# Kernel optimization log

Hardware: AMD Instinct MI355X
Metric: run time of the kernel (lower is better)

The kernel has to match this reference:

```python
import jax, jax.numpy as jnp
import numpy as np

D_MODEL = 1024
NUM_HEADS = 16
HEAD_DIM = D_MODEL // NUM_HEADS
FFN_HIDDEN = 4096
EPS = 1e-5


def setup_inputs() -> dict:
    key = jax.random.key(0)
    ks = jax.random.split(key, 7)
    s = 0.02
    return {
        "x": jax.random.normal(ks[0], (2, 2048, D_MODEL), dtype=jnp.float32),
        "W_qkv": jax.random.normal(ks[1], (D_MODEL, 3 * D_MODEL), dtype=jnp.float32) * s,
        "b_qkv": jnp.zeros((3 * D_MODEL,), dtype=jnp.float32),
        "W_o": jax.random.normal(ks[2], (D_MODEL, D_MODEL), dtype=jnp.float32) * s,
        "b_o": jnp.zeros((D_MODEL,), dtype=jnp.float32),
        "gamma1": jnp.ones((D_MODEL,), dtype=jnp.float32),
        "beta1": jnp.zeros((D_MODEL,), dtype=jnp.float32),
        "W1": jax.random.normal(ks[3], (D_MODEL, FFN_HIDDEN), dtype=jnp.float32) * s,
        "b1": jnp.zeros((FFN_HIDDEN,), dtype=jnp.float32),
        "W2": jax.random.normal(ks[4], (FFN_HIDDEN, D_MODEL), dtype=jnp.float32) * s,
        "b2": jnp.zeros((D_MODEL,), dtype=jnp.float32),
        "gamma2": jnp.ones((D_MODEL,), dtype=jnp.float32),
        "beta2": jnp.zeros((D_MODEL,), dtype=jnp.float32),
    }


def _layernorm(x, gamma, beta):
    mean = jnp.mean(x, axis=-1, keepdims=True)
    var = jnp.mean((x - mean) ** 2, axis=-1, keepdims=True)
    return gamma * (x - mean) / jnp.sqrt(var + EPS) + beta


def reference(x, W_qkv, b_qkv, W_o, b_o, gamma1, beta1, W1, b1, W2, b2, gamma2, beta2):
    B, S, D = x.shape
    # ---- multi-head attention ----
    qkv = x @ W_qkv + b_qkv                       # [B,S,3D]
    qkv = qkv.reshape(B, S, NUM_HEADS, 3 * HEAD_DIM).transpose(0, 2, 1, 3)  # [B,H,S,3hd]
    q, k, v = jnp.split(qkv, 3, axis=-1)          # each [B,H,S,hd]
    scores = jnp.einsum("bhqd,bhkd->bhqk", q, k) / np.sqrt(HEAD_DIM)
    attn = jax.nn.softmax(scores, axis=-1)
    vals = jnp.einsum("bhqk,bhkd->bhqd", attn, v)
    vals = vals.transpose(0, 2, 1, 3).reshape(B, S, D)
    attn_out = vals @ W_o + b_o
    # dropout disabled (eval mode)
    h = _layernorm(attn_out + x, gamma1, beta1)
    # ---- position-wise FFN (dropout before relu per source, disabled) ----
    ffn = jax.nn.relu(h @ W1 + b1) @ W2 + b2
    return _layernorm(ffn + h, gamma2, beta2)
```

## Files before the change

kernel.cpp:

```cpp
#include <hip/hip_runtime.h>
#include <stdint.h>

typedef float v4f __attribute__((ext_vector_type(4)));
typedef __bf16 v8bf __attribute__((ext_vector_type(8)));
typedef __bf16 v4bf __attribute__((ext_vector_type(4)));
typedef unsigned short v8us __attribute__((ext_vector_type(8)));
typedef unsigned short v4us __attribute__((ext_vector_type(4)));

__device__ __forceinline__ float b2f(unsigned short u) {
    union { float f; uint32_t i; } x; x.i = ((uint32_t)u) << 16; return x.f;
}
__device__ __forceinline__ unsigned short f2b(float f) {
    union { float f; uint32_t u; } x; x.f = f;
    uint32_t r = x.u + 0x7fffu + ((x.u >> 16) & 1u);
    return (unsigned short)(r >> 16);
}

__device__ __forceinline__ void gload16(const unsigned short* g, unsigned short* l) {
    __builtin_amdgcn_global_load_lds(
        (const __attribute__((address_space(1))) void*)g,
        (__attribute__((address_space(3))) void*)l,
        16, 0, 0);
}

__device__ __forceinline__ void transpose_tile(
    const float* __restrict__ W, unsigned short* __restrict__ WT,
    int K, int N, int kb, int nb, int tid)
{
    __shared__ unsigned short t[64][65];
    const int r = tid >> 4, c4 = (tid & 15) * 4;
    #pragma unroll
    for (int i = 0; i < 4; ++i) {
        int k = r + i * 16;
        float4 v = *(const float4*)&W[(size_t)(kb + k) * N + nb + c4];
        t[c4 + 0][k] = f2b(v.x);
        t[c4 + 1][k] = f2b(v.y);
        t[c4 + 2][k] = f2b(v.z);
        t[c4 + 3][k] = f2b(v.w);
    }
    __syncthreads();
    #pragma unroll
    for (int i = 0; i < 4; ++i) {
        int n = r + i * 16;
        v4us o = {t[n][c4], t[n][c4 + 1], t[n][c4 + 2], t[n][c4 + 3]};
        *(v4us*)&WT[(size_t)(nb + n) * K + kb + c4] = o;
    }
}

__global__ __launch_bounds__(256) void prep_fused(
    const float* __restrict__ x, unsigned short* __restrict__ xb,
    const float* __restrict__ Wqkv, unsigned short* __restrict__ WqkvT,
    const float* __restrict__ W1, unsigned short* __restrict__ W1T,
    const float* __restrict__ Wo, unsigned short* __restrict__ WoT)
{
    const int b = blockIdx.x, tid = threadIdx.x;
    if (b < 4096) {
        int i = (b * 256 + tid) * 4;
        float4 v = *(const float4*)&x[i];
        v4us o = {f2b(v.x), f2b(v.y), f2b(v.z), f2b(v.w)};
        *(v4us*)&xb[i] = o;
    } else if (b < 4096 + 768) {
        int lb = b - 4096;
        transpose_tile(Wqkv, WqkvT, 1024, 3072, (lb / 48) * 64, (lb % 48) * 64, tid);
    } else if (b < 4096 + 768 + 1024) {
        int lb = b - 4096 - 768;
        transpose_tile(W1, W1T, 1024, 4096, (lb / 64) * 64, (lb % 64) * 64, tid);
    } else {
        int lb = b - 4096 - 768 - 1024;
        transpose_tile(Wo, WoT, 1024, 1024, (lb / 16) * 64, (lb % 16) * 64, tid);
    }
}

__device__ __forceinline__ void xcd_swizzle(int& bm, int& bn) {
    int NB = gridDim.x, MB = gridDim.y;
    int flat = blockIdx.x + NB * blockIdx.y;
    int xcd = flat & 7, j = flat >> 3;
    int MBand = MB >> 3;
    bm = xcd * MBand + (j % MBand);
    bn = j / MBand;
}

__global__ __launch_bounds__(256) void gemm_bt_n64(
    const unsigned short* __restrict__ A, const unsigned short* __restrict__ BT,
    const float* __restrict__ bias, unsigned short* __restrict__ C,
    int M, int N, int K, int relu)
{
    __shared__ __align__(16) unsigned short sA0[2][128 * 32];
    __shared__ __align__(16) unsigned short sB0[2][64 * 32];
    __shared__ __align__(16) unsigned short sA1[2][128 * 32];
    __shared__ __align__(16) unsigned short sB1[2][64 * 32];
    const int tid  = threadIdx.x;
    const int wave = tid >> 6, lane = tid & 63;
    const int wm = wave >> 1, wn = wave & 1;
    const int quad = lane >> 4, l16 = lane & 15;
    int bm, bn;
    xcd_swizzle(bm, bn);

    const int srow = lane >> 2, scol = (lane & 3) * 8;
    const unsigned short* ga0 = A  + (size_t)(bm * 128 + (wave * 2 + 0) * 16 + srow) * K + scol;
    const unsigned short* ga1 = A  + (size_t)(bm * 128 + (wave * 2 + 1) * 16 + srow) * K + scol;
    const unsigned short* gb0 = BT + (size_t)(bn * 64 + wave * 16 + srow) * K + scol;
    const int oa0 = (wave * 2 + 0) * 512 + lane * 8;
    const int oa1 = (wave * 2 + 1) * 512 + lane * 8;
    const int ob  = wave * 512 + lane * 8;

    v8us aR0[2][2], bR0[2], aR1[2][2], bR1[2];
    #pragma unroll
    for (int c = 0; c < 2; ++c) {
        aR0[c][0] = *(const v8us*)(ga0 + c * 32);
        aR0[c][1] = *(const v8us*)(ga1 + c * 32);
        bR0[c]    = *(const v8us*)(gb0 + c * 32);
        aR1[c][0] = *(const v8us*)(ga0 + 64 + c * 32);
        aR1[c][1] = *(const v8us*)(ga1 + 64 + c * 32);
        bR1[c]    = *(const v8us*)(gb0 + 64 + c * 32);
    }

    v4f acc[4][2];
    #pragma unroll
    for (int i = 0; i < 4; ++i)
        #pragma unroll
        for (int j = 0; j < 2; ++j)
            acc[i][j] = (v4f){0.f, 0.f, 0.f, 0.f};

    for (int kt = 0; kt < K; kt += 128) {
        #pragma unroll
        for (int c = 0; c < 2; ++c) {
            *(v8us*)&sA0[c][oa0] = aR0[c][0];
            *(v8us*)&sA0[c][oa1] = aR0[c][1];
            *(v8us*)&sB0[c][ob]  = bR0[c];
        }
        __syncthreads();
        if (kt + 128 < K) {
            const int kn = kt + 128;
            #pragma unroll
            for (int c = 0; c < 2; ++c) {
                aR0[c][0] = *(const v8us*)(ga0 + kn + c * 32);
                aR0[c][1] = *(const v8us*)(ga1 + kn + c * 32);
                bR0[c]    = *(const v8us*)(gb0 + kn + c * 32);
            }
        }
        #pragma unroll
        for (int c = 0; c < 2; ++c) {
            v8bf af[4], bfr[2];
            #pragma unroll
            for (int mt = 0; mt < 4; ++mt)
                af[mt] = *(const v8bf*)&sA0[c][(wm * 64 + mt * 16 + l16) * 32 + quad * 8];
            #pragma unroll
            for (int nt = 0; nt < 2; ++nt)
                bfr[nt] = *(const v8bf*)&sB0[c][(wn * 32 + nt * 16 + l16) * 32 + quad * 8];
            #pragma unroll
            for (int mt = 0; mt < 4; ++mt)
                #pragma unroll
                for (int nt = 0; nt < 2; ++nt)
                    acc[mt][nt] = __builtin_amdgcn_mfma_f32_16x16x32_bf16(
                        af[mt], bfr[nt], acc[mt][nt], 0, 0, 0);
        }

        #pragma unroll
        for (int c = 0; c < 2; ++c) {
            *(v8us*)&sA1[c][oa0] = aR1[c][0];
            *(v8us*)&sA1[c][oa1] = aR1[c][1];
            *(v8us*)&sB1[c][ob]  = bR1[c];
        }
        __syncthreads();
        if (kt + 192 < K) {
            const int kn = kt + 192;
            #pragma unroll
            for (int c = 0; c < 2; ++c) {
                aR1[c][0] = *(const v8us*)(ga0 + kn + c * 32);
                aR1[c][1] = *(const v8us*)(ga1 + kn + c * 32);
                bR1[c]    = *(const v8us*)(gb0 + kn + c * 32);
            }
        }
        #pragma unroll
        for (int c = 0; c < 2; ++c) {
            v8bf af[4], bfr[2];
            #pragma unroll
            for (int mt = 0; mt < 4; ++mt)
                af[mt] = *(const v8bf*)&sA1[c][(wm * 64 + mt * 16 + l16) * 32 + quad * 8];
            #pragma unroll
            for (int nt = 0; nt < 2; ++nt)
                bfr[nt] = *(const v8bf*)&sB1[c][(wn * 32 + nt * 16 + l16) * 32 + quad * 8];
            #pragma unroll
            for (int mt = 0; mt < 4; ++mt)
                #pragma unroll
                for (int nt = 0; nt < 2; ++nt)
                    acc[mt][nt] = __builtin_amdgcn_mfma_f32_16x16x32_bf16(
                        af[mt], bfr[nt], acc[mt][nt], 0, 0, 0);
        }
    }

    #pragma unroll
    for (int mt = 0; mt < 4; ++mt) {
        #pragma unroll
        for (int nt = 0; nt < 2; ++nt) {
            int col = bn * 64 + wn * 32 + nt * 16 + l16;
            float bv = bias ? bias[col] : 0.f;
            #pragma unroll
            for (int r = 0; r < 4; ++r) {
                int row = bm * 128 + wm * 64 + mt * 16 + quad * 4 + r;
                float v = acc[mt][nt][r] + bv;
                if (relu) v = fmaxf(v, 0.f);
                C[(size_t)row * N + col] = f2b(v);
            }
        }
    }
}

template<int SPLIT_V>
__global__ __launch_bounds__(512) void gemm256(
    const unsigned short* __restrict__ A, const unsigned short* __restrict__ BT,
    const float* __restrict__ bias, unsigned short* __restrict__ C,
    unsigned short* __restrict__ VT, int M, int N, int K, int relu)
{
    __shared__ __align__(16) unsigned short sA[2][256 * 64];
    __shared__ __align__(16) unsigned short sB[2][256 * 64];
    const int tid  = threadIdx.x;
    const int wave = tid >> 6, lane = tid & 63;
    const int wm = wave >> 2, wn = wave & 3;
    const int quad = lane >> 4, l16 = lane & 15;
    int bm, bn;
    xcd_swizzle(bm, bn);

    const int srow = lane >> 3;
    const int scol = ((lane & 7) * 8) ^ ((lane & 32) ? 16 : 0);
    size_t aoff[4], boff[4];
    #pragma unroll
    for (int j = 0; j < 4; ++j) {
        int r = wave * 32 + j * 8 + srow;
        aoff[j] = (size_t)(bm * 256 + r) * K + scol;
        boff[j] = (size_t)(bn * 256 + r) * K + scol;
    }
    const int lds0 = wave * 32 * 64;

    const int ksw = (quad * 8) ^ ((l16 & 4) ? 16 : 0);

    v4f acc[8][4];
    #pragma unroll
    for (int i = 0; i < 8; ++i)
        #pragma unroll
        for (int j = 0; j < 4; ++j)
            acc[i][j] = (v4f){0.f, 0.f, 0.f, 0.f};

    const int NT = K >> 6;
    #pragma unroll
    for (int j = 0; j < 4; ++j) {
        gload16(A  + aoff[j], &sA[0][lds0 + j * 512]);
        gload16(BT + boff[j], &sB[0][lds0 + j * 512]);
    }
    __syncthreads();

    for (int t = 0; t < NT; ++t) {
        const int buf = t & 1;
        if (t + 1 < NT) {
            const int ktn = (t + 1) << 6;
            #pragma unroll
            for (int j = 0; j < 4; ++j) {
                gload16(A  + aoff[j] + ktn, &sA[buf ^ 1][lds0 + j * 512]);
                gload16(BT + boff[j] + ktn, &sB[buf ^ 1][lds0 + j * 512]);
            }
        }

        v8bf bfr[4][2];
        #pragma unroll
        for (int nt2 = 0; nt2 < 4; ++nt2)
            #pragma unroll
            for (int kc = 0; kc < 2; ++kc)
                bfr[nt2][kc] = *(const v8bf*)&sB[buf][
                    (wn * 64 + nt2 * 16 + l16) * 64 + kc * 32 + ksw];
        #pragma unroll
        for (int mq = 0; mq < 2; ++mq) {
            v8bf af[4][2];
            #pragma unroll
            for (int mt2 = 0; mt2 < 4; ++mt2)
                #pragma unroll
                for (int kc = 0; kc < 2; ++kc)
                    af[mt2][kc] = *(const v8bf*)&sA[buf][
                        (wm * 128 + mq * 64 + mt2 * 16 + l16) * 64 + kc * 32 + ksw];
            #pragma unroll
            for (int mt2 = 0; mt2 < 4; ++mt2)
                #pragma unroll
                for (int nt2 = 0; nt2 < 4; ++nt2)
                    #pragma unroll
                    for (int kc = 0; kc < 2; ++kc)
                        acc[mq * 4 + mt2][nt2] =
                            __builtin_amdgcn_mfma_f32_16x16x32_bf16(
                                af[mt2][kc], bfr[nt2][kc],
                                acc[mq * 4 + mt2][nt2], 0, 0, 0);
        }
        __syncthreads();
    }

    #pragma unroll
    for (int mt = 0; mt < 8; ++mt) {
        int row = bm * 256 + wm * 128 + mt * 16 + quad * 4;
        #pragma unroll
        for (int nt = 0; nt < 4; ++nt) {
            int c0 = bn * 256 + wn * 64 + nt * 16;
            int col = c0 + l16;
            float bv = bias ? bias[col] : 0.f;
            if (SPLIT_V && (c0 % 192) >= 128) {
                int hh = c0 / 192;
                int d  = (c0 % 192) - 128 + l16;
                int bb = row >> 11;
                int s  = row & 2047;
                v4us st;
                #pragma unroll
                for (int r = 0; r < 4; ++r)
                    st[r] = f2b(acc[mt][nt][r] + bv);
                *(v4us*)&VT[((size_t)(bb * 16 + hh) * 64 + d) * 2048 + s] = st;
            } else {
                float qs = (SPLIT_V && (c0 % 192) < 64) ? 0.18033688f : 1.0f;
                #pragma unroll
                for (int r = 0; r < 4; ++r) {
                    float v = (acc[mt][nt][r] + bv) * qs;
                    if (relu) v = fmaxf(v, 0.f);
                    C[(size_t)(row + r) * N + col] = f2b(v);
                }
            }
        }
    }
}

__global__ __launch_bounds__(512) void attn_mfma(
    const unsigned short* __restrict__ qkv, const unsigned short* __restrict__ VT,
    unsigned short* __restrict__ av)
{
    __shared__ __align__(16) unsigned short sK[2][64 * 72];
    __shared__ __align__(16) unsigned short sVT[2][64 * 72];
    __shared__ __align__(16) unsigned short sP[8][16 * 72];
    const int tid  = threadIdx.x;
    const int wave = tid >> 6, lane = tid & 63;
    const int quad = lane >> 4, l16 = lane & 15;
    const int blk = blockIdx.x;
    const int xcd = blk & 7, local = blk >> 3;
    const int bh = xcd * 4 + (local & 3);
    const int qb = local >> 2;
    const int h = bh & 15, b = bh >> 4;
    const int row0 = b * 2048;
    const int qbase = row0 + qb * 128 + wave * 16;
    const size_t qoff = (size_t)h * 192;
    const size_t koff = qoff + 64;

    v8bf qf[2];
    #pragma unroll
    for (int kc = 0; kc < 2; ++kc)
        qf[kc] = *(const v8bf*)&qkv[(size_t)(qbase + l16) * 3072
                                    + qoff + kc * 32 + quad * 8];

    v4f o[4];
    #pragma unroll
    for (int dt = 0; dt < 4; ++dt)
        o[dt] = (v4f){0.f, 0.f, 0.f, 0.f};
    float ll = 0.f;

    const int k_key = tid >> 3, k_oct = (tid & 7) * 8;
    const unsigned short* gK = qkv + (size_t)(row0 + k_key) * 3072 + koff + k_oct;
    const unsigned short* gV = VT + ((size_t)bh * 64 + k_key) * 2048 + k_oct;
    const size_t stepK = (size_t)64 * 3072;
    const size_t stepV = 64;

    v8us kreg = *(const v8us*)gK;
    v8us vreg = *(const v8us*)gV;
    gK += stepK; gV += stepV;

    for (int kt = 0; kt < 32; ++kt) {
        const int cur = kt & 1;
        *(v8us*)&sK[cur][k_key * 72 + k_oct]  = kreg;
        *(v8us*)&sVT[cur][k_key * 72 + k_oct] = vreg;
        __syncthreads();
        if (kt < 31) {
            kreg = *(const v8us*)gK;
            vreg = *(const v8us*)gV;
            gK += stepK; gV += stepV;
        }

        v4f sc[4];
        #pragma unroll
        for (int kk = 0; kk < 4; ++kk) {
            sc[kk] = (v4f){0.f, 0.f, 0.f, 0.f};
            #pragma unroll
            for (int kc = 0; kc < 2; ++kc) {
                v8bf ak = *(const v8bf*)&sK[cur][(kk * 16 + l16) * 72 + kc * 32 + quad * 8];
                sc[kk] = __builtin_amdgcn_mfma_f32_16x16x32_bf16(
                    ak, qf[kc], sc[kk], 0, 0, 0);
            }
        }

        float ps = 0.f;
        #pragma unroll
        for (int kk = 0; kk < 4; ++kk) {
            v4bf pk;
            #pragma unroll
            for (int rr = 0; rr < 4; ++rr) {
                float p = __builtin_amdgcn_exp2f(sc[kk][rr]);
                ps += p;
                pk[rr] = (__bf16)p;
            }
            *(v4bf*)&sP[wave][l16 * 72 + kk * 16 + quad * 4] = pk;
        }
        ll += ps;

        __asm__ volatile("s_waitcnt lgkmcnt(0)" ::: "memory");

        #pragma unroll
        for (int c = 0; c < 2; ++c) {
            union { v8bf v; v8us u; } u;
            u.u = *(const v8us*)&sP[wave][l16 * 72 + c * 32 + quad * 8];
            v8bf pb = u.v;
            #pragma unroll
            for (int dt = 0; dt < 4; ++dt) {
                v8bf va = *(const v8bf*)&sVT[cur][(dt * 16 + l16) * 72 + c * 32 + quad * 8];
                o[dt] = __builtin_amdgcn_mfma_f32_16x16x32_bf16(
                    va, pb, o[dt], 0, 0, 0);
            }
        }
    }

    float l = ll;
    l += __shfl_xor(l, 16, 64);
    l += __shfl_xor(l, 32, 64);
    float inv = 1.f / l;
    int qrow = qbase + l16;
    #pragma unroll
    for (int dt = 0; dt < 4; ++dt) {
        v4bf st;
        #pragma unroll
        for (int rr = 0; rr < 4; ++rr)
            st[rr] = (__bf16)(o[dt][rr] * inv);
        *(v4bf*)&av[(size_t)qrow * 1024 + h * 64 + dt * 16 + quad * 4] = st;
    }
}

__device__ __forceinline__ void ln_row_f32res(
    const unsigned short* __restrict__ a, const float* __restrict__ resid,
    const float* __restrict__ gamma, const float* __restrict__ beta,
    unsigned short* __restrict__ outp, int row, int tid)
{
    const size_t base = (size_t)row * 1024;
    const int c0 = tid * 4;
    ushort4 avv = *(const ushort4*)&a[base + c0];
    float4 rv = *(const float4*)&resid[base + c0];
    float y[4];
    y[0] = b2f(avv.x) + rv.x;
    y[1] = b2f(avv.y) + rv.y;
    y[2] = b2f(avv.z) + rv.z;
    y[3] = b2f(avv.w) + rv.w;
    float s  = y[0] + y[1] + y[2] + y[3];
    float ss = y[0]*y[0] + y[1]*y[1] + y[2]*y[2] + y[3]*y[3];
    #pragma unroll
    for (int off = 32; off; off >>= 1) {
        s  += __shfl_xor(s, off, 64);
        ss += __shfl_xor(ss, off, 64);
    }
    __shared__ float red[8];
    int wave = tid >> 6, lane = tid & 63;
    if (lane == 0) { red[wave] = s; red[4 + wave] = ss; }
    __syncthreads();
    s  = red[0] + red[1] + red[2] + red[3];
    ss = red[4] + red[5] + red[6] + red[7];
    float mean = s * (1.f / 1024.f);
    float var  = ss * (1.f / 1024.f) - mean * mean;
    float rstd = rsqrtf(var + 1e-5f);
    float4 gv = *(const float4*)&gamma[c0];
    float4 bv = *(const float4*)&beta[c0];
    ushort4 ov;
    ov.x = f2b(gv.x * (y[0] - mean) * rstd + bv.x);
    ov.y = f2b(gv.y * (y[1] - mean) * rstd + bv.y);
    ov.z = f2b(gv.z * (y[2] - mean) * rstd + bv.z);
    ov.w = f2b(gv.w * (y[3] - mean) * rstd + bv.w);
    *(ushort4*)&outp[base + c0] = ov;
}

__global__ __launch_bounds__(256) void ln1_w2t_fused(
    const unsigned short* __restrict__ a, const float* __restrict__ x,
    const float* __restrict__ gamma, const float* __restrict__ beta,
    unsigned short* __restrict__ h_out,
    const float* __restrict__ W2, unsigned short* __restrict__ W2T)
{
    const int b = blockIdx.x, tid = threadIdx.x;
    if (b < 4096) {
        ln_row_f32res(a, x, gamma, beta, h_out, b, tid);
    } else {
        int lb = b - 4096;
        transpose_tile(W2, W2T, 4096, 1024, (lb / 16) * 64, (lb % 16) * 64, tid);
    }
}

template<int RES_F32, int OUT_F32>
__global__ __launch_bounds__(256) void ln_fused(
    const unsigned short* __restrict__ a, const void* __restrict__ residv,
    const float* __restrict__ gamma, const float* __restrict__ beta,
    void* __restrict__ outv)
{
    const int row = blockIdx.x, tid = threadIdx.x;
    const size_t base = (size_t)row * 1024;
    const int c0 = tid * 4;
    ushort4 avv = *(const ushort4*)&a[base + c0];
    float y[4];
    if (RES_F32) {
        float4 rv = *(const float4*)((const float*)residv + base + c0);
        y[0] = b2f(avv.x) + rv.x;
        y[1] = b2f(avv.y) + rv.y;
        y[2] = b2f(avv.z) + rv.z;
        y[3] = b2f(avv.w) + rv.w;
    } else {
        ushort4 rv = *(const ushort4*)((const unsigned short*)residv + base + c0);
        y[0] = b2f(avv.x) + b2f(rv.x);
        y[1] = b2f(avv.y) + b2f(rv.y);
        y[2] = b2f(avv.z) + b2f(rv.z);
        y[3] = b2f(avv.w) + b2f(rv.w);
    }
    float s  = y[0] + y[1] + y[2] + y[3];
    float ss = y[0]*y[0] + y[1]*y[1] + y[2]*y[2] + y[3]*y[3];
    #pragma unroll
    for (int off = 32; off; off >>= 1) {
        s  += __shfl_xor(s, off, 64);
        ss += __shfl_xor(ss, off, 64);
    }
    __shared__ float red[8];
    int wave = tid >> 6, lane = tid & 63;
    if (lane == 0) { red[wave] = s; red[4 + wave] = ss; }
    __syncthreads();
    s  = red[0] + red[1] + red[2] + red[3];
    ss = red[4] + red[5] + red[6] + red[7];
    float mean = s * (1.f / 1024.f);
    float var  = ss * (1.f / 1024.f) - mean * mean;
    float rstd = rsqrtf(var + 1e-5f);
    float4 gv = *(const float4*)&gamma[c0];
    float4 bv = *(const float4*)&beta[c0];
    float r0 = gv.x * (y[0] - mean) * rstd + bv.x;
    float r1 = gv.y * (y[1] - mean) * rstd + bv.y;
    float r2 = gv.z * (y[2] - mean) * rstd + bv.z;
    float r3 = gv.w * (y[3] - mean) * rstd + bv.w;
    if (OUT_F32) {
        float4 ov = {r0, r1, r2, r3};
        *(float4*)((float*)outv + base + c0) = ov;
    } else {
        ushort4 ov;
        ov.x = f2b(r0); ov.y = f2b(r1); ov.z = f2b(r2); ov.w = f2b(r3);
        *(ushort4*)((unsigned short*)outv + base + c0) = ov;
    }
}

extern "C" void kernel_launch(void* const* d_in, const int* in_sizes, int n_in,
                              void* d_out, int out_size, void* d_ws, size_t ws_size,
                              hipStream_t stream)
{
    (void)in_sizes; (void)n_in; (void)out_size; (void)ws_size;
    const float* x    = (const float*)d_in[0];
    const float* Wqkv = (const float*)d_in[1];
    const float* bqkv = (const float*)d_in[2];
    const float* Wo   = (const float*)d_in[3];
    const float* bo   = (const float*)d_in[4];
    const float* g1   = (const float*)d_in[5];
    const float* be1  = (const float*)d_in[6];
    const float* W1   = (const float*)d_in[7];
    const float* b1   = (const float*)d_in[8];
    const float* W2   = (const float*)d_in[9];
    const float* b2   = (const float*)d_in[10];
    const float* g2   = (const float*)d_in[11];
    const float* be2  = (const float*)d_in[12];
    float* out = (float*)d_out;

    unsigned short* R0 = (unsigned short*)d_ws;
    unsigned short* R1 = R0 + (size_t)16 * 1024 * 1024;
    unsigned short* R2 = R1 + (size_t)4 * 1024 * 1024;
    unsigned short* R3 = R2 + (size_t)4 * 1024 * 1024;
    unsigned short* WqkvT = R0 + (size_t)12 * 1024 * 1024;
    unsigned short* WoT   = R0 + (size_t)15 * 1024 * 1024;

    const int M = 4096;
    dim3 blk(256);

    prep_fused<<<dim3(4096 + 768 + 1024 + 256), blk, 0, stream>>>(
        x, R2, Wqkv, WqkvT, W1, R3, Wo, WoT);
    gemm256<1><<<dim3(12, 16), dim3(512), 0, stream>>>(R2, WqkvT, bqkv, R0, R1, M, 3072, 1024, 0);
    attn_mfma<<<dim3(512), dim3(512), 0, stream>>>(R0, R1, R2);
    gemm_bt_n64<<<dim3(16, 32), blk, 0, stream>>>(R2, WoT, bo, R1, M, 1024, 1024, 0);
    ln1_w2t_fused<<<dim3(4096 + 1024), blk, 0, stream>>>(R1, x, g1, be1, R1, W2, R2);
    gemm256<0><<<dim3(16, 16), dim3(512), 0, stream>>>(R1, R3, b1, R0, nullptr, M, 4096, 1024, 1);
    gemm_bt_n64<<<dim3(16, 32), blk, 0, stream>>>(R0, R2, b2, R3, M, 1024, 4096, 0);
    ln_fused<0, 1><<<dim3(4096), blk, 0, stream>>>(R3, R1, g2, be2, out);
}
```

Measured before the change: 338.2 us.

## Replace 256x256 double-buffered GEMM with 128x128 single-buffered tiles

Shrinks the QKV and FFN1 GEMM tiles from 256x256 with 512 threads to 128x128 with 256 threads. It also drops the LDS double buffering in favour of a simple load-sync-compute loop. The goal is more blocks (768 and 1024 instead of 192 and 256) to fill the 256 CUs better, with less LDS and register pressure per block. In exchange, per-block data reuse is lower and global-to-LDS loads are no longer overlapped with MFMA work inside a block.

Result: slower. 354.6 us (+4.8%).

```diff
diff --git a/kernel.cpp b/kernel.cpp
--- a/kernel.cpp
+++ b/kernel.cpp
@@ -208,16 +208,16 @@
 }
 
 template<int SPLIT_V>
-__global__ __launch_bounds__(512) void gemm256(
+__global__ __launch_bounds__(256) void gemm128(
     const unsigned short* __restrict__ A, const unsigned short* __restrict__ BT,
     const float* __restrict__ bias, unsigned short* __restrict__ C,
     unsigned short* __restrict__ VT, int M, int N, int K, int relu)
 {
-    __shared__ __align__(16) unsigned short sA[2][256 * 64];
-    __shared__ __align__(16) unsigned short sB[2][256 * 64];
+    __shared__ __align__(16) unsigned short sA[128 * 64];
+    __shared__ __align__(16) unsigned short sB[128 * 64];
     const int tid  = threadIdx.x;
     const int wave = tid >> 6, lane = tid & 63;
-    const int wm = wave >> 2, wn = wave & 3;
+    const int wm = wave >> 1, wn = wave & 1;
     const int quad = lane >> 4, l16 = lane & 15;
     int bm, bn;
     xcd_swizzle(bm, bn);
@@ -228,75 +228,59 @@
     #pragma unroll
     for (int j = 0; j < 4; ++j) {
         int r = wave * 32 + j * 8 + srow;
-        aoff[j] = (size_t)(bm * 256 + r) * K + scol;
-        boff[j] = (size_t)(bn * 256 + r) * K + scol;
+        aoff[j] = (size_t)(bm * 128 + r) * K + scol;
+        boff[j] = (size_t)(bn * 128 + r) * K + scol;
     }
     const int lds0 = wave * 32 * 64;
 
     const int ksw = (quad * 8) ^ ((l16 & 4) ? 16 : 0);
 
-    v4f acc[8][4];
-    #pragma unroll
-    for (int i = 0; i < 8; ++i)
+    v4f acc[4][4];
+    #pragma unroll
+    for (int i = 0; i < 4; ++i)
         #pragma unroll
         for (int j = 0; j < 4; ++j)
             acc[i][j] = (v4f){0.f, 0.f, 0.f, 0.f};
 
-    const int NT = K >> 6;
-    #pragma unroll
-    for (int j = 0; j < 4; ++j) {
-        gload16(A  + aoff[j], &sA[0][lds0 + j * 512]);
-        gload16(BT + boff[j], &sB[0][lds0 + j * 512]);
-    }
-    __syncthreads();
-
-    for (int t = 0; t < NT; ++t) {
-        const int buf = t & 1;
-        if (t + 1 < NT) {
-            const int ktn = (t + 1) << 6;
-            #pragma unroll
-            for (int j = 0; j < 4; ++j) {
-                gload16(A  + aoff[j] + ktn, &sA[buf ^ 1][lds0 + j * 512]);
-                gload16(BT + boff[j] + ktn, &sB[buf ^ 1][lds0 + j * 512]);
-            }
-        }
-
-        v8bf bfr[4][2];
-        #pragma unroll
-        for (int nt2 = 0; nt2 < 4; ++nt2)
+    for (int kt = 0; kt < K; kt += 64) {
+        __syncthreads();
+        #pragma unroll
+        for (int j = 0; j < 4; ++j)
+            gload16(A  + aoff[j] + kt, &sA[lds0 + j * 512]);
+        #pragma unroll
+        for (int j = 0; j < 4; ++j)
+            gload16(BT + boff[j] + kt, &sB[lds0 + j * 512]);
+        __syncthreads();
+
+        v8bf af[4][2], bfr[4][2];
+        #pragma unroll
+        for (int mt = 0; mt < 4; ++mt)
             #pragma unroll
             for (int kc = 0; kc < 2; ++kc)
-                bfr[nt2][kc] = *(const v8bf*)&sB[buf][
-                    (wn * 64 + nt2 * 16 + l16) * 64 + kc * 32 + ksw];
-        #pragma unroll
-        for (int mq = 0; mq < 2; ++mq) {
-            v8bf af[4][2];
-            #pragma unroll
-            for (int mt2 = 0; mt2 < 4; ++mt2)
+                af[mt][kc] = *(const v8bf*)&sA[
+                    (wm * 64 + mt * 16 + l16) * 64 + kc * 32 + ksw];
+        #pragma unroll
+        for (int nt = 0; nt < 4; ++nt)
+            #pragma unroll
+            for (int kc = 0; kc < 2; ++kc)
+                bfr[nt][kc] = *(const v8bf*)&sB[
+                    (wn * 64 + nt * 16 + l16) * 64 + kc * 32 + ksw];
+        #pragma unroll
+        for (int mt = 0; mt < 4; ++mt)
+            #pragma unroll
+            for (int nt = 0; nt < 4; ++nt)
                 #pragma unroll
                 for (int kc = 0; kc < 2; ++kc)
-                    af[mt2][kc] = *(const v8bf*)&sA[buf][
-                        (wm * 128 + mq * 64 + mt2 * 16 + l16) * 64 + kc * 32 + ksw];
-            #pragma unroll
-            for (int mt2 = 0; mt2 < 4; ++mt2)
-                #pragma unroll
-                for (int nt2 = 0; nt2 < 4; ++nt2)
-                    #pragma unroll
-                    for (int kc = 0; kc < 2; ++kc)
-                        acc[mq * 4 + mt2][nt2] =
-                            __builtin_amdgcn_mfma_f32_16x16x32_bf16(
-                                af[mt2][kc], bfr[nt2][kc],
-                                acc[mq * 4 + mt2][nt2], 0, 0, 0);
-        }
-        __syncthreads();
-    }
-
-    #pragma unroll
-    for (int mt = 0; mt < 8; ++mt) {
-        int row = bm * 256 + wm * 128 + mt * 16 + quad * 4;
+                    acc[mt][nt] = __builtin_amdgcn_mfma_f32_16x16x32_bf16(
+                        af[mt][kc], bfr[nt][kc], acc[mt][nt], 0, 0, 0);
+    }
+
+    #pragma unroll
+    for (int mt = 0; mt < 4; ++mt) {
+        int row = bm * 128 + wm * 64 + mt * 16 + quad * 4;
         #pragma unroll
         for (int nt = 0; nt < 4; ++nt) {
-            int c0 = bn * 256 + wn * 64 + nt * 16;
+            int c0 = bn * 128 + wn * 64 + nt * 16;
             int col = c0 + l16;
             float bv = bias ? bias[col] : 0.f;
             if (SPLIT_V && (c0 % 192) >= 128) {
@@ -575,11 +559,11 @@
 
     prep_fused<<<dim3(4096 + 768 + 1024 + 256), blk, 0, stream>>>(
         x, R2, Wqkv, WqkvT, W1, R3, Wo, WoT);
-    gemm256<1><<<dim3(12, 16), dim3(512), 0, stream>>>(R2, WqkvT, bqkv, R0, R1, M, 3072, 1024, 0);
+    gemm128<1><<<dim3(24, 32), blk, 0, stream>>>(R2, WqkvT, bqkv, R0, R1, M, 3072, 1024, 0);
     attn_mfma<<<dim3(512), dim3(512), 0, stream>>>(R0, R1, R2);
     gemm_bt_n64<<<dim3(16, 32), blk, 0, stream>>>(R2, WoT, bo, R1, M, 1024, 1024, 0);
     ln1_w2t_fused<<<dim3(4096 + 1024), blk, 0, stream>>>(R1, x, g1, be1, R1, W2, R2);
-    gemm256<0><<<dim3(16, 16), dim3(512), 0, stream>>>(R1, R3, b1, R0, nullptr, M, 4096, 1024, 1);
+    gemm128<0><<<dim3(32, 32), blk, 0, stream>>>(R1, R3, b1, R0, nullptr, M, 4096, 1024, 1);
     gemm_bt_n64<<<dim3(16, 32), blk, 0, stream>>>(R0, R2, b2, R3, M, 1024, 4096, 0);
     ln_fused<0, 1><<<dim3(4096), blk, 0, stream>>>(R3, R1, g2, be2, out);
 }
```
